# Optimization experiments

Hardware: AMD Instinct MI355X
Metric: run time of the kernel (lower is better)

The kernel has to match this reference:

```python
import jax, jax.numpy as jnp
import numpy as np

N = 50000      # nodes
E = 800000     # edges (avg degree 16)
IN_DIM = 128
H = 64         # hidden (GINSmall default)
C = 2          # n_classes
G = 64         # number of graphs in batch


def setup_inputs() -> dict:
    key = jax.random.key(0)
    ks = jax.random.split(key, 16)
    s = 0.05
    inp = {
        "x": jax.random.normal(ks[0], (N, IN_DIM), dtype=jnp.float32),
        "edge_index": jax.random.randint(ks[1], (2, E), 0, N, dtype=jnp.int64),
        "batch": jnp.sort(jax.random.randint(ks[2], (N,), 0, G, dtype=jnp.int64)),
        # conv 0 MLP
        "W1_0": jax.random.normal(ks[3], (IN_DIM, H), dtype=jnp.float32) * s,
        "b1_0": jnp.zeros((H,), jnp.float32),
        "W2_0": jax.random.normal(ks[4], (H, H), dtype=jnp.float32) * s,
        "b2_0": jnp.zeros((H,), jnp.float32),
        # conv 1 MLP
        "W1_1": jax.random.normal(ks[5], (H, H), dtype=jnp.float32) * s,
        "b1_1": jnp.zeros((H,), jnp.float32),
        "W2_1": jax.random.normal(ks[6], (H, H), dtype=jnp.float32) * s,
        "b2_1": jnp.zeros((H,), jnp.float32),
        # conv 2 MLP
        "W1_2": jax.random.normal(ks[7], (H, H), dtype=jnp.float32) * s,
        "b1_2": jnp.zeros((H,), jnp.float32),
        "W2_2": jax.random.normal(ks[8], (H, H), dtype=jnp.float32) * s,
        "b2_2": jnp.zeros((H,), jnp.float32),
        # readout
        "Wl": jax.random.normal(ks[9], (H, C), dtype=jnp.float32) * s,
        "bl": jnp.zeros((C,), jnp.float32),
    }
    return inp


def _gin_conv(h, src, dst, W1, b1, W2, b2):
    # GINConv with eps=0: MLP(h_i + sum_{j->i} h_j)
    agg = jax.ops.segment_sum(h[src], dst, num_segments=N)  # [N, d]
    z = h + agg
    return jnp.maximum(z @ W1 + b1, 0.0) @ W2 + b2


def reference(x, edge_index, batch,
              W1_0, b1_0, W2_0, b2_0,
              W1_1, b1_1, W2_1, b2_1,
              W1_2, b1_2, W2_2, b2_2,
              Wl, bl):
    src, dst = edge_index[0], edge_index[1]  # PyG: messages flow src -> dst
    params = [(W1_0, b1_0, W2_0, b2_0),
              (W1_1, b1_1, W2_1, b2_1),
              (W1_2, b1_2, W2_2, b2_2)]
    h = x
    for (W1, b1, W2, b2) in params:
        h = _gin_conv(h, src, dst, W1, b1, W2, b2)
        h = jnp.maximum(h, 0.0)  # ReLU; dropout is identity at inference
    # global mean pool over graph ids
    sums = jax.ops.segment_sum(h, batch, num_segments=G)          # [G, H]
    cnt = jax.ops.segment_sum(jnp.ones((N,), h.dtype), batch, num_segments=G)
    g = sums / jnp.maximum(cnt, 1.0)[:, None]
    out = g @ Wl + bl
    return out, g
```

## Files before the change

kernel.cpp:

```cpp
#include <hip/hip_runtime.h>

typedef unsigned short ushort_t;
typedef __attribute__((ext_vector_type(8))) short short8;
typedef __attribute__((ext_vector_type(4))) float f32x4;

__device__ inline float bflo(unsigned int u) { return __uint_as_float(u << 16); }
__device__ inline float bfhi(unsigned int u) { return __uint_as_float(u & 0xFFFF0000u); }
__device__ inline unsigned short f2bf(float f) {
    unsigned int u = __float_as_uint(f);
    return (unsigned short)((u + 0x7FFFu + ((u >> 16) & 1u)) >> 16);
}
__device__ inline unsigned int pk(float a, float b) {
    return (unsigned int)f2bf(a) | ((unsigned int)f2bf(b) << 16);
}

union U16B { uint4 u; short8 s; };

#define HB 512

__global__ __launch_bounds__(256) void gemm_hist(const float* __restrict__ x,
                                                 const float* __restrict__ W1,
                                                 ushort_t* __restrict__ Y, int n,
                                                 const int* __restrict__ dst,
                                                 int* __restrict__ deg,
                                                 int* __restrict__ rank, int E) {
    if (blockIdx.x < HB) {
        for (int e = blockIdx.x * 256 + threadIdx.x; e < E; e += HB * 256)
            rank[e] = atomicAdd(&deg[dst[e]], 1);
        return;
    }
    __shared__ ushort_t w1f[4][4][64][8];
    __shared__ ushort_t ybuf[64][72];
    for (int i = threadIdx.x; i < 8192; i += 256) {
        int j = i & 7, lane = (i >> 3) & 63, ct = (i >> 9) & 3, ks = (i >> 11) & 3;
        int k = ks * 32 + ((lane >> 4) << 3) + j;
        int c = ct * 16 + (lane & 15);
        w1f[ks][ct][lane][j] = f2bf(W1[k * 64 + c]);
    }
    __syncthreads();
    int w = threadIdx.x >> 6, lane = threadIdx.x & 63;
    int row0 = (blockIdx.x - HB) * 64;
    int arow = row0 + w * 16 + (lane & 15);
    if (arow >= n) arow = n - 1;
    const float* xr = x + (size_t)arow * 128;
    int k0base = (lane >> 4) << 3;

    f32x4 acc[4] = {{0,0,0,0},{0,0,0,0},{0,0,0,0},{0,0,0,0}};
#pragma unroll
    for (int ks = 0; ks < 4; ks++) {
        int k0 = ks * 32 + k0base;
        float4 aa = *(const float4*)(xr + k0);
        float4 ab = *(const float4*)(xr + k0 + 4);
        U16B af;
        af.u.x = pk(aa.x, aa.y);
        af.u.y = pk(aa.z, aa.w);
        af.u.z = pk(ab.x, ab.y);
        af.u.w = pk(ab.z, ab.w);
#pragma unroll
        for (int ct = 0; ct < 4; ct++) {
            short8 bf = *(const short8*)&w1f[ks][ct][lane][0];
            acc[ct] = __builtin_amdgcn_mfma_f32_16x16x32_bf16(af.s, bf, acc[ct], 0, 0, 0);
        }
    }
#pragma unroll
    for (int ct = 0; ct < 4; ct++)
#pragma unroll
        for (int r = 0; r < 4; r++)
            ybuf[w * 16 + ((lane >> 4) << 2) + r][ct * 16 + (lane & 15)] = f2bf(acc[ct][r]);
    __syncthreads();
    int row = threadIdx.x >> 2, seg = threadIdx.x & 3;
    if (row0 + row < n) {
        const uint4* p = (const uint4*)&ybuf[row][seg * 16];
        uint4 v0 = p[0], v1 = p[1];
        uint4* q = (uint4*)(Y + (size_t)(row0 + row) * 64 + seg * 16);
        q[0] = v0; q[1] = v1;
    }
}

__global__ __launch_bounds__(256) void scan_all(const int* __restrict__ deg,
                                                int* __restrict__ rowptr,
                                                int* __restrict__ aggr,
                                                int* __restrict__ flags, int n) {
    __shared__ int sdata[256];
    __shared__ int sagg[64];
    int b = blockIdx.x;
    int t = threadIdx.x;
    int base = b * 1024 + t * 4;
    int v[4]; int s = 0;
#pragma unroll
    for (int k = 0; k < 4; k++) { int i = base + k; v[k] = (i < n) ? deg[i] : 0; s += v[k]; }
    sdata[t] = s;
    __syncthreads();
    for (int off = 1; off < 256; off <<= 1) {
        int x = 0;
        if (t >= off) x = sdata[t - off];
        __syncthreads();
        if (t >= off) sdata[t] += x;
        __syncthreads();
    }
    int ex = sdata[t] - s;
    if (t == 255) {
        aggr[b] = sdata[255];
        __threadfence();
        atomicExch(&flags[b], 1);
    }
    if (t < 64) { while (atomicAdd(&flags[t], 0) == 0) {} }
    __syncthreads();
    if (t < 64) sagg[t] = aggr[t];
    __syncthreads();
    int bp = 0;
    for (int i = 0; i < b; i++) bp += sagg[i];
    int off = bp + ex;
#pragma unroll
    for (int k = 0; k < 4; k++) {
        int i = base + k;
        if (i < n) { rowptr[i] = off; off += v[k]; }
    }
    if (b == 63 && t == 255) rowptr[n] = bp + sdata[255];
}

__global__ __launch_bounds__(256) void fill_range(const int* __restrict__ src,
                                                  const int* __restrict__ dst,
                                                  const int* __restrict__ rank,
                                                  const int* __restrict__ rowptr,
                                                  int* __restrict__ col, int E, int CE) {
    int range = blockIdx.x & 7;
    int sub = blockIdx.x >> 3;
    int e0 = sub * CE;
    int e1 = min(e0 + CE, E);
    for (int e = e0 + threadIdx.x; e < e1; e += 256) {
        int d = dst[e];
        if ((d >> 13) == range) col[rowptr[d] + rank[e]] = src[e];
    }
}

template <int HASNEXT>
__global__ __launch_bounds__(256) void gfuse(const ushort_t* __restrict__ Y,
                                             const int* __restrict__ rowptr,
                                             const int* __restrict__ col,
                                             const float* __restrict__ b1,
                                             const float* __restrict__ W2,
                                             const float* __restrict__ b2,
                                             const float* __restrict__ Wn,
                                             ushort_t* __restrict__ Yn,
                                             const int* __restrict__ batch,
                                             float* __restrict__ sums, int n) {
    __shared__ ushort_t w2f[2][4][64][8];
    __shared__ ushort_t wnf[HASNEXT ? 2 : 1][4][64][8];
    __shared__ ushort_t st[64][72];
    __shared__ float vbuf[HASNEXT ? 1 : 64][65];
    __shared__ float b1s[64], b2s[64];
    for (int i = threadIdx.x; i < 4096; i += 256) {
        int j = i & 7, lane = (i >> 3) & 63, ct = (i >> 9) & 3, ks = (i >> 11) & 1;
        int k = ks * 32 + ((lane >> 4) << 3) + j;
        int c = ct * 16 + (lane & 15);
        w2f[ks][ct][lane][j] = f2bf(W2[k * 64 + c]);
        if (HASNEXT) wnf[ks][ct][lane][j] = f2bf(Wn[k * 64 + c]);
    }
    if (threadIdx.x < 64) { b1s[threadIdx.x] = b1[threadIdx.x]; b2s[threadIdx.x] = b2[threadIdx.x]; }
    __syncthreads();

    int row0 = blockIdx.x * 64;

    {
        int lr = threadIdx.x >> 2;
        int q  = threadIdx.x & 3;
        int gnode = row0 + lr;
        uint4 o0, o1;
        if (gnode < n) {
            const ushort_t* yb = Y + (size_t)gnode * 64 + q * 16;
            uint4 v0 = *(const uint4*)yb;
            uint4 v1 = *(const uint4*)(yb + 8);
            float ga[16];
            ga[0]=bflo(v0.x); ga[1]=bfhi(v0.x); ga[2]=bflo(v0.y); ga[3]=bfhi(v0.y);
            ga[4]=bflo(v0.z); ga[5]=bfhi(v0.z); ga[6]=bflo(v0.w); ga[7]=bfhi(v0.w);
            ga[8]=bflo(v1.x); ga[9]=bfhi(v1.x); ga[10]=bflo(v1.y); ga[11]=bfhi(v1.y);
            ga[12]=bflo(v1.z); ga[13]=bfhi(v1.z); ga[14]=bflo(v1.w); ga[15]=bfhi(v1.w);
            int e = rowptr[gnode], e1 = rowptr[gnode + 1];
            while (e + 1 < e1) {
                const ushort_t* p0 = Y + (size_t)col[e] * 64 + q * 16;
                const ushort_t* p1 = Y + (size_t)col[e + 1] * 64 + q * 16;
                uint4 a0 = *(const uint4*)p0, a1 = *(const uint4*)(p0 + 8);
                uint4 c0 = *(const uint4*)p1, c1 = *(const uint4*)(p1 + 8);
                ga[0]+=bflo(a0.x)+bflo(c0.x); ga[1]+=bfhi(a0.x)+bfhi(c0.x);
                ga[2]+=bflo(a0.y)+bflo(c0.y); ga[3]+=bfhi(a0.y)+bfhi(c0.y);
                ga[4]+=bflo(a0.z)+bflo(c0.z); ga[5]+=bfhi(a0.z)+bfhi(c0.z);
                ga[6]+=bflo(a0.w)+bflo(c0.w); ga[7]+=bfhi(a0.w)+bfhi(c0.w);
                ga[8]+=bflo(a1.x)+bflo(c1.x); ga[9]+=bfhi(a1.x)+bfhi(c1.x);
                ga[10]+=bflo(a1.y)+bflo(c1.y); ga[11]+=bfhi(a1.y)+bfhi(c1.y);
                ga[12]+=bflo(a1.z)+bflo(c1.z); ga[13]+=bfhi(a1.z)+bfhi(c1.z);
                ga[14]+=bflo(a1.w)+bflo(c1.w); ga[15]+=bfhi(a1.w)+bfhi(c1.w);
                e += 2;
            }
            if (e < e1) {
                const ushort_t* p0 = Y + (size_t)col[e] * 64 + q * 16;
                uint4 a0 = *(const uint4*)p0, a1 = *(const uint4*)(p0 + 8);
                ga[0]+=bflo(a0.x); ga[1]+=bfhi(a0.x); ga[2]+=bflo(a0.y); ga[3]+=bfhi(a0.y);
                ga[4]+=bflo(a0.z); ga[5]+=bfhi(a0.z); ga[6]+=bflo(a0.w); ga[7]+=bfhi(a0.w);
                ga[8]+=bflo(a1.x); ga[9]+=bfhi(a1.x); ga[10]+=bflo(a1.y); ga[11]+=bfhi(a1.y);
                ga[12]+=bflo(a1.z); ga[13]+=bfhi(a1.z); ga[14]+=bflo(a1.w); ga[15]+=bfhi(a1.w);
            }
            int d0 = q * 16;
#pragma unroll
            for (int j = 0; j < 16; j++) ga[j] = fmaxf(ga[j] + b1s[d0 + j], 0.0f);
            o0.x = pk(ga[0], ga[1]);  o0.y = pk(ga[2], ga[3]);
            o0.z = pk(ga[4], ga[5]);  o0.w = pk(ga[6], ga[7]);
            o1.x = pk(ga[8], ga[9]);  o1.y = pk(ga[10], ga[11]);
            o1.z = pk(ga[12], ga[13]); o1.w = pk(ga[14], ga[15]);
        } else {
            o0 = make_uint4(0, 0, 0, 0); o1 = o0;
        }
        *(uint4*)&st[lr][q * 16] = o0;
        *(uint4*)&st[lr][q * 16 + 8] = o1;
    }
    __syncthreads();

    int w = threadIdx.x >> 6, lane = threadIdx.x & 63;
    int k0base = (lane >> 4) << 3;
    f32x4 acc[4] = {{0,0,0,0},{0,0,0,0},{0,0,0,0},{0,0,0,0}};
#pragma unroll
    for (int ks = 0; ks < 2; ks++) {
        short8 af = *(const short8*)&st[w * 16 + (lane & 15)][ks * 32 + k0base];
#pragma unroll
        for (int ct = 0; ct < 4; ct++) {
            short8 bf = *(const short8*)&w2f[ks][ct][lane][0];
            acc[ct] = __builtin_amdgcn_mfma_f32_16x16x32_bf16(af, bf, acc[ct], 0, 0, 0);
        }
    }
    __syncthreads();

    int colb = lane & 15;
    if (HASNEXT) {
#pragma unroll
        for (int ct = 0; ct < 4; ct++)
#pragma unroll
            for (int r = 0; r < 4; r++) {
                float v = fmaxf(acc[ct][r] + b2s[ct * 16 + colb], 0.0f);
                st[w * 16 + ((lane >> 4) << 2) + r][ct * 16 + colb] = f2bf(v);
            }
        __syncthreads();
        f32x4 acc2[4] = {{0,0,0,0},{0,0,0,0},{0,0,0,0},{0,0,0,0}};
#pragma unroll
        for (int ks = 0; ks < 2; ks++) {
            short8 af2 = *(const short8*)&st[w * 16 + (lane & 15)][ks * 32 + k0base];
#pragma unroll
            for (int ct = 0; ct < 4; ct++) {
                short8 bf = *(const short8*)&wnf[ks][ct][lane][0];
                acc2[ct] = __builtin_amdgcn_mfma_f32_16x16x32_bf16(af2, bf, acc2[ct], 0, 0, 0);
            }
        }
        __syncthreads();
#pragma unroll
        for (int ct = 0; ct < 4; ct++)
#pragma unroll
            for (int r = 0; r < 4; r++)
                st[w * 16 + ((lane >> 4) << 2) + r][ct * 16 + colb] = f2bf(acc2[ct][r]);
        __syncthreads();
        int row = threadIdx.x >> 2, seg = threadIdx.x & 3;
        if (row0 + row < n) {
            const uint4* p = (const uint4*)&st[row][seg * 16];
            uint4 v0 = p[0], v1 = p[1];
            uint4* qp = (uint4*)(Yn + (size_t)(row0 + row) * 64 + seg * 16);
            qp[0] = v0; qp[1] = v1;
        }
    } else {
#pragma unroll
        for (int ct = 0; ct < 4; ct++)
#pragma unroll
            for (int r = 0; r < 4; r++) {
                float v = fmaxf(acc[ct][r] + b2s[ct * 16 + colb], 0.0f);
                vbuf[w * 16 + ((lane >> 4) << 2) + r][ct * 16 + colb] = v;
            }
        __syncthreads();
        int j  = threadIdx.x & 63;
        int i0 = (threadIdx.x >> 6) * 16;
        int cur = -1; float a = 0.0f;
        for (int i = i0; i < i0 + 16; i++) {
            int row = row0 + i;
            if (row >= n) break;
            int b = batch[row];
            if (b != cur) {
                if (cur >= 0) atomicAdd(&sums[cur * 64 + j], a);
                cur = b; a = 0.0f;
            }
            a += vbuf[i][j];
        }
        if (cur >= 0) atomicAdd(&sums[cur * 64 + j], a);
    }
}

__global__ __launch_bounds__(64) void finalize_kernel(const float* __restrict__ sums,
                                                      const int* __restrict__ batch, int n,
                                                      const float* __restrict__ Wl,
                                                      const float* __restrict__ bl,
                                                      float* __restrict__ out, int G) {
    int g = blockIdx.x;
    int j = threadIdx.x;
    __shared__ float gs[64];
    int lo = 0, hi = n;
    while (lo < hi) { int m = (lo + hi) >> 1; if (batch[m] < g) lo = m + 1; else hi = m; }
    int lo2 = lo, hi2 = n;
    while (lo2 < hi2) { int m = (lo2 + hi2) >> 1; if (batch[m] < g + 1) lo2 = m + 1; else hi2 = m; }
    float c = (float)max(lo2 - lo, 1);
    float v = sums[g * 64 + j] / c;
    gs[j] = v;
    out[G * 2 + g * 64 + j] = v;
    __syncthreads();
    if (j < 2) {
        float acc = bl[j];
#pragma unroll
        for (int k = 0; k < 64; k++) acc += gs[k] * Wl[k * 2 + j];
        out[g * 2 + j] = acc;
    }
}

extern "C" void kernel_launch(void* const* d_in, const int* in_sizes, int n_in,
                              void* d_out, int out_size, void* d_ws, size_t ws_size,
                              hipStream_t stream) {
    const float* x     = (const float*)d_in[0];
    const int*   ei    = (const int*)d_in[1];
    const int*   batch = (const int*)d_in[2];
    const float* W1_0 = (const float*)d_in[3];
    const float* b1_0 = (const float*)d_in[4];
    const float* W2_0 = (const float*)d_in[5];
    const float* b2_0 = (const float*)d_in[6];
    const float* W1_1 = (const float*)d_in[7];
    const float* b1_1 = (const float*)d_in[8];
    const float* W2_1 = (const float*)d_in[9];
    const float* b2_1 = (const float*)d_in[10];
    const float* W1_2 = (const float*)d_in[11];
    const float* b1_2 = (const float*)d_in[12];
    const float* W2_2 = (const float*)d_in[13];
    const float* b2_2 = (const float*)d_in[14];
    const float* Wl   = (const float*)d_in[15];
    const float* bl   = (const float*)d_in[16];

    const int N = in_sizes[0] / 128;
    const int E = in_sizes[1] / 2;
    const int G = out_size / 66;
    const int* src = ei;
    const int* dst = ei + E;
    float* out = (float*)d_out;

    ushort_t* Y   = (ushort_t*)d_ws;
    ushort_t* Y2  = Y + (size_t)N * 64;
    float* sums   = (float*)(Y2 + (size_t)N * 64);
    int*   deg    = (int*)(sums + (size_t)G * 64);
    int*   flags  = deg + N;
    int*   rowptr = flags + 64;
    int*   col    = rowptr + (N + 1);
    int*   rank   = col + E;
    int*   aggr   = rank + E;

    hipMemsetAsync(sums, 0, ((size_t)G * 64 + N + 64) * sizeof(int), stream);

    const int mblk = (N + 63) / 64;

    gemm_hist<<<HB + mblk, 256, 0, stream>>>(x, W1_0, Y, N, dst, deg, rank, E);
    scan_all<<<64, 256, 0, stream>>>(deg, rowptr, aggr, flags, N);
    const int SUBS = 64;
    const int CE = (E + SUBS - 1) / SUBS;
    fill_range<<<8 * SUBS, 256, 0, stream>>>(src, dst, rank, rowptr, col, E, CE);

    gfuse<1><<<mblk, 256, 0, stream>>>(Y, rowptr, col, b1_0, W2_0, b2_0, W1_1, Y2, nullptr, nullptr, N);
    gfuse<1><<<mblk, 256, 0, stream>>>(Y2, rowptr, col, b1_1, W2_1, b2_1, W1_2, Y, nullptr, nullptr, N);
    gfuse<0><<<mblk, 256, 0, stream>>>(Y, rowptr, col, b1_2, W2_2, b2_2, nullptr, nullptr, batch, sums, N);
    finalize_kernel<<<G, 64, 0, stream>>>(sums, batch, N, Wl, bl, out, G);
}
```

Before: 173.9 us.

## Partition CSR neighbor lists by source half to localize gather accesses

```diff
diff --git a/kernel.cpp b/kernel.cpp
--- a/kernel.cpp
+++ b/kernel.cpp
@@ -21,12 +21,16 @@
 __global__ __launch_bounds__(256) void gemm_hist(const float* __restrict__ x,
                                                  const float* __restrict__ W1,
                                                  ushort_t* __restrict__ Y, int n,
+                                                 const int* __restrict__ src,
                                                  const int* __restrict__ dst,
                                                  int* __restrict__ deg,
-                                                 int* __restrict__ rank, int E) {
+                                                 int* __restrict__ rank, int E, int HALF) {
     if (blockIdx.x < HB) {
-        for (int e = blockIdx.x * 256 + threadIdx.x; e < E; e += HB * 256)
-            rank[e] = atomicAdd(&deg[dst[e]], 1);
+        for (int e = blockIdx.x * 256 + threadIdx.x; e < E; e += HB * 256) {
+            int d = dst[e];
+            int off = (src[e] >= HALF) ? n : 0;
+            rank[e] = atomicAdd(&deg[d + off], 1);
+        }
         return;
     }
     __shared__ ushort_t w1f[4][4][64][8];
@@ -88,7 +92,11 @@
     int base = b * 1024 + t * 4;
     int v[4]; int s = 0;
 #pragma unroll
-    for (int k = 0; k < 4; k++) { int i = base + k; v[k] = (i < n) ? deg[i] : 0; s += v[k]; }
+    for (int k = 0; k < 4; k++) {
+        int i = base + k;
+        v[k] = (i < n) ? deg[i] + deg[n + i] : 0;
+        s += v[k];
+    }
     sdata[t] = s;
     __syncthreads();
     for (int off = 1; off < 256; off <<= 1) {
@@ -123,14 +131,19 @@
                                                   const int* __restrict__ dst,
                                                   const int* __restrict__ rank,
                                                   const int* __restrict__ rowptr,
-                                                  int* __restrict__ col, int E, int CE) {
+                                                  const int* __restrict__ deg,
+                                                  int* __restrict__ col, int E, int CE, int HALF) {
     int range = blockIdx.x & 7;
     int sub = blockIdx.x >> 3;
     int e0 = sub * CE;
     int e1 = min(e0 + CE, E);
     for (int e = e0 + threadIdx.x; e < e1; e += 256) {
         int d = dst[e];
-        if ((d >> 13) == range) col[rowptr[d] + rank[e]] = src[e];
+        if ((d >> 13) == range) {
+            int s = src[e];
+            int base = rowptr[d] + ((s >= HALF) ? deg[d] : 0);
+            col[base + rank[e]] = s;
+        }
     }
 }
 
@@ -138,6 +151,7 @@
 __global__ __launch_bounds__(256) void gfuse(const ushort_t* __restrict__ Y,
                                              const int* __restrict__ rowptr,
                                              const int* __restrict__ col,
+                                             const int* __restrict__ degA,
                                              const float* __restrict__ b1,
                                              const float* __restrict__ W2,
                                              const float* __restrict__ b2,
@@ -176,29 +190,35 @@
             ga[4]=bflo(v0.z); ga[5]=bfhi(v0.z); ga[6]=bflo(v0.w); ga[7]=bfhi(v0.w);
             ga[8]=bflo(v1.x); ga[9]=bfhi(v1.x); ga[10]=bflo(v1.y); ga[11]=bfhi(v1.y);
             ga[12]=bflo(v1.z); ga[13]=bfhi(v1.z); ga[14]=bflo(v1.w); ga[15]=bfhi(v1.w);
-            int e = rowptr[gnode], e1 = rowptr[gnode + 1];
-            while (e + 1 < e1) {
-                const ushort_t* p0 = Y + (size_t)col[e] * 64 + q * 16;
-                const ushort_t* p1 = Y + (size_t)col[e + 1] * 64 + q * 16;
-                uint4 a0 = *(const uint4*)p0, a1 = *(const uint4*)(p0 + 8);
-                uint4 c0 = *(const uint4*)p1, c1 = *(const uint4*)(p1 + 8);
-                ga[0]+=bflo(a0.x)+bflo(c0.x); ga[1]+=bfhi(a0.x)+bfhi(c0.x);
-                ga[2]+=bflo(a0.y)+bflo(c0.y); ga[3]+=bfhi(a0.y)+bfhi(c0.y);
-                ga[4]+=bflo(a0.z)+bflo(c0.z); ga[5]+=bfhi(a0.z)+bfhi(c0.z);
-                ga[6]+=bflo(a0.w)+bflo(c0.w); ga[7]+=bfhi(a0.w)+bfhi(c0.w);
-                ga[8]+=bflo(a1.x)+bflo(c1.x); ga[9]+=bfhi(a1.x)+bfhi(c1.x);
-                ga[10]+=bflo(a1.y)+bflo(c1.y); ga[11]+=bfhi(a1.y)+bfhi(c1.y);
-                ga[12]+=bflo(a1.z)+bflo(c1.z); ga[13]+=bfhi(a1.z)+bfhi(c1.z);
-                ga[14]+=bflo(a1.w)+bflo(c1.w); ga[15]+=bfhi(a1.w)+bfhi(c1.w);
-                e += 2;
-            }
-            if (e < e1) {
-                const ushort_t* p0 = Y + (size_t)col[e] * 64 + q * 16;
-                uint4 a0 = *(const uint4*)p0, a1 = *(const uint4*)(p0 + 8);
-                ga[0]+=bflo(a0.x); ga[1]+=bfhi(a0.x); ga[2]+=bflo(a0.y); ga[3]+=bfhi(a0.y);
-                ga[4]+=bflo(a0.z); ga[5]+=bfhi(a0.z); ga[6]+=bflo(a0.w); ga[7]+=bfhi(a0.w);
-                ga[8]+=bflo(a1.x); ga[9]+=bfhi(a1.x); ga[10]+=bflo(a1.y); ga[11]+=bfhi(a1.y);
-                ga[12]+=bflo(a1.z); ga[13]+=bfhi(a1.z); ga[14]+=bflo(a1.w); ga[15]+=bfhi(a1.w);
+            int r0 = rowptr[gnode], r1 = rowptr[gnode + 1];
+            int sp = r0 + degA[gnode];
+#pragma unroll 1
+            for (int p = 0; p < 2; p++) {
+                int e  = p ? sp : r0;
+                int ed = p ? r1 : sp;
+                while (e + 1 < ed) {
+                    const ushort_t* p0 = Y + (size_t)col[e] * 64 + q * 16;
+                    const ushort_t* p1 = Y + (size_t)col[e + 1] * 64 + q * 16;
+                    uint4 a0 = *(const uint4*)p0, a1 = *(const uint4*)(p0 + 8);
+                    uint4 c0 = *(const uint4*)p1, c1 = *(const uint4*)(p1 + 8);
+                    ga[0]+=bflo(a0.x)+bflo(c0.x); ga[1]+=bfhi(a0.x)+bfhi(c0.x);
+                    ga[2]+=bflo(a0.y)+bflo(c0.y); ga[3]+=bfhi(a0.y)+bfhi(c0.y);
+                    ga[4]+=bflo(a0.z)+bflo(c0.z); ga[5]+=bfhi(a0.z)+bfhi(c0.z);
+                    ga[6]+=bflo(a0.w)+bflo(c0.w); ga[7]+=bfhi(a0.w)+bfhi(c0.w);
+                    ga[8]+=bflo(a1.x)+bflo(c1.x); ga[9]+=bfhi(a1.x)+bfhi(c1.x);
+                    ga[10]+=bflo(a1.y)+bflo(c1.y); ga[11]+=bfhi(a1.y)+bfhi(c1.y);
+                    ga[12]+=bflo(a1.z)+bflo(c1.z); ga[13]+=bfhi(a1.z)+bfhi(c1.z);
+                    ga[14]+=bflo(a1.w)+bflo(c1.w); ga[15]+=bfhi(a1.w)+bfhi(c1.w);
+                    e += 2;
+                }
+                if (e < ed) {
+                    const ushort_t* p0 = Y + (size_t)col[e] * 64 + q * 16;
+                    uint4 a0 = *(const uint4*)p0, a1 = *(const uint4*)(p0 + 8);
+                    ga[0]+=bflo(a0.x); ga[1]+=bfhi(a0.x); ga[2]+=bflo(a0.y); ga[3]+=bfhi(a0.y);
+                    ga[4]+=bflo(a0.z); ga[5]+=bfhi(a0.z); ga[6]+=bflo(a0.w); ga[7]+=bfhi(a0.w);
+                    ga[8]+=bflo(a1.x); ga[9]+=bfhi(a1.x); ga[10]+=bflo(a1.y); ga[11]+=bfhi(a1.y);
+                    ga[12]+=bflo(a1.z); ga[13]+=bfhi(a1.z); ga[14]+=bflo(a1.w); ga[15]+=bfhi(a1.w);
+                }
             }
             int d0 = q * 16;
 #pragma unroll
@@ -341,29 +361,30 @@
     const int* src = ei;
     const int* dst = ei + E;
     float* out = (float*)d_out;
+    const int HALF = N / 2;
 
     ushort_t* Y   = (ushort_t*)d_ws;
     ushort_t* Y2  = Y + (size_t)N * 64;
     float* sums   = (float*)(Y2 + (size_t)N * 64);
     int*   deg    = (int*)(sums + (size_t)G * 64);
-    int*   flags  = deg + N;
+    int*   flags  = deg + 2 * (size_t)N;
     int*   rowptr = flags + 64;
     int*   col    = rowptr + (N + 1);
     int*   rank   = col + E;
     int*   aggr   = rank + E;
 
-    hipMemsetAsync(sums, 0, ((size_t)G * 64 + N + 64) * sizeof(int), stream);
+    hipMemsetAsync(sums, 0, ((size_t)G * 64 + 2 * (size_t)N + 64) * sizeof(int), stream);
 
     const int mblk = (N + 63) / 64;
 
-    gemm_hist<<<HB + mblk, 256, 0, stream>>>(x, W1_0, Y, N, dst, deg, rank, E);
+    gemm_hist<<<HB + mblk, 256, 0, stream>>>(x, W1_0, Y, N, src, dst, deg, rank, E, HALF);
     scan_all<<<64, 256, 0, stream>>>(deg, rowptr, aggr, flags, N);
     const int SUBS = 64;
     const int CE = (E + SUBS - 1) / SUBS;
-    fill_range<<<8 * SUBS, 256, 0, stream>>>(src, dst, rank, rowptr, col, E, CE);
-
-    gfuse<1><<<mblk, 256, 0, stream>>>(Y, rowptr, col, b1_0, W2_0, b2_0, W1_1, Y2, nullptr, nullptr, N);
-    gfuse<1><<<mblk, 256, 0, stream>>>(Y2, rowptr, col, b1_1, W2_1, b2_1, W1_2, Y, nullptr, nullptr, N);
-    gfuse<0><<<mblk, 256, 0, stream>>>(Y, rowptr, col, b1_2, W2_2, b2_2, nullptr, nullptr, batch, sums, N);
+    fill_range<<<8 * SUBS, 256, 0, stream>>>(src, dst, rank, rowptr, deg, col, E, CE, HALF);
+
+    gfuse<1><<<mblk, 256, 0, stream>>>(Y, rowptr, col, deg, b1_0, W2_0, b2_0, W1_1, Y2, nullptr, nullptr, N);
+    gfuse<1><<<mblk, 256, 0, stream>>>(Y2, rowptr, col, deg, b1_1, W2_1, b2_1, W1_2, Y, nullptr, nullptr, N);
+    gfuse<0><<<mblk, 256, 0, stream>>>(Y, rowptr, col, deg, b1_2, W2_2, b2_2, nullptr, nullptr, batch, sums, N);
     finalize_kernel<<<G, 64, 0, stream>>>(sums, batch, N, Wl, bl, out, G);
 }
```

Result: slower. 186.0 us (+6.9%).

## Fuse CSR scan and column fill into one kernel with flag-based handoff

Applied to the files above, without the earlier changes.

```diff
diff --git a/kernel.cpp b/kernel.cpp
--- a/kernel.cpp
+++ b/kernel.cpp
@@ -17,6 +17,7 @@
 union U16B { uint4 u; short8 s; };
 
 #define HB 512
+#define SUBS 192
 
 __global__ __launch_bounds__(256) void gemm_hist(const float* __restrict__ x,
                                                  const float* __restrict__ W1,
@@ -77,60 +78,71 @@
     }
 }
 
-__global__ __launch_bounds__(256) void scan_all(const int* __restrict__ deg,
-                                                int* __restrict__ rowptr,
-                                                int* __restrict__ aggr,
-                                                int* __restrict__ flags, int n) {
-    __shared__ int sdata[256];
-    __shared__ int sagg[64];
-    int b = blockIdx.x;
+__global__ __launch_bounds__(256) void scan_fill(const int* __restrict__ deg,
+                                                 int* __restrict__ rowptr,
+                                                 int* __restrict__ aggr,
+                                                 int* __restrict__ flags,
+                                                 int* __restrict__ flags2,
+                                                 const int* __restrict__ src,
+                                                 const int* __restrict__ dst,
+                                                 const int* __restrict__ rank,
+                                                 int* __restrict__ col,
+                                                 int n, int E, int CE, int RB) {
     int t = threadIdx.x;
-    int base = b * 1024 + t * 4;
-    int v[4]; int s = 0;
-#pragma unroll
-    for (int k = 0; k < 4; k++) { int i = base + k; v[k] = (i < n) ? deg[i] : 0; s += v[k]; }
-    sdata[t] = s;
-    __syncthreads();
-    for (int off = 1; off < 256; off <<= 1) {
-        int x = 0;
-        if (t >= off) x = sdata[t - off];
-        __syncthreads();
-        if (t >= off) sdata[t] += x;
-        __syncthreads();
-    }
-    int ex = sdata[t] - s;
-    if (t == 255) {
-        aggr[b] = sdata[255];
+    if (blockIdx.x < 64) {
+        __shared__ int sdata[256];
+        __shared__ int sagg[64];
+        int b = blockIdx.x;
+        int base = b * 1024 + t * 4;
+        int v[4]; int s = 0;
+#pragma unroll
+        for (int k = 0; k < 4; k++) { int i = base + k; v[k] = (i < n) ? deg[i] : 0; s += v[k]; }
+        sdata[t] = s;
+        __syncthreads();
+        for (int off = 1; off < 256; off <<= 1) {
+            int x = 0;
+            if (t >= off) x = sdata[t - off];
+            __syncthreads();
+            if (t >= off) sdata[t] += x;
+            __syncthreads();
+        }
+        int ex = sdata[t] - s;
+        if (t == 255) {
+            aggr[b] = sdata[255];
+            __threadfence();
+            atomicExch(&flags[b], 1);
+        }
+        if (t < 64) { while (atomicAdd(&flags[t], 0) == 0) {} }
+        __syncthreads();
+        if (t < 64) sagg[t] = aggr[t];
+        __syncthreads();
+        int bp = 0;
+        for (int i = 0; i < b; i++) bp += sagg[i];
+        int off = bp + ex;
+#pragma unroll
+        for (int k = 0; k < 4; k++) {
+            int i = base + k;
+            if (i < n) { rowptr[i] = off; off += v[k]; }
+        }
+        if (b == 63 && t == 255) rowptr[n] = bp + sdata[255];
+        __syncthreads();
         __threadfence();
-        atomicExch(&flags[b], 1);
-    }
-    if (t < 64) { while (atomicAdd(&flags[t], 0) == 0) {} }
-    __syncthreads();
-    if (t < 64) sagg[t] = aggr[t];
-    __syncthreads();
-    int bp = 0;
-    for (int i = 0; i < b; i++) bp += sagg[i];
-    int off = bp + ex;
-#pragma unroll
-    for (int k = 0; k < 4; k++) {
-        int i = base + k;
-        if (i < n) { rowptr[i] = off; off += v[k]; }
-    }
-    if (b == 63 && t == 255) rowptr[n] = bp + sdata[255];
-}
-
-__global__ __launch_bounds__(256) void fill_range(const int* __restrict__ src,
-                                                  const int* __restrict__ dst,
-                                                  const int* __restrict__ rank,
-                                                  const int* __restrict__ rowptr,
-                                                  int* __restrict__ col, int E, int CE) {
-    int range = blockIdx.x & 7;
-    int sub = blockIdx.x >> 3;
-    int e0 = sub * CE;
-    int e1 = min(e0 + CE, E);
-    for (int e = e0 + threadIdx.x; e < e1; e += 256) {
-        int d = dst[e];
-        if ((d >> 13) == range) col[rowptr[d] + rank[e]] = src[e];
+        if (t == 0) atomicExch(&flags2[b], 1);
+    } else {
+        if (t < 64) { while (atomicAdd(&flags2[t], 0) == 0) {} }
+        __syncthreads();
+        int fb = blockIdx.x - 64;
+        int range = fb & 7;
+        int sub = fb >> 3;
+        int e0 = sub * CE;
+        int e1 = min(e0 + CE, E);
+        int lo = range * RB;
+        int hi = lo + RB;
+#pragma unroll 4
+        for (int e = e0 + t; e < e1; e += 256) {
+            int d = dst[e];
+            if (d >= lo && d < hi) col[rowptr[d] + rank[e]] = src[e];
+        }
     }
 }
 
@@ -347,20 +359,21 @@
     float* sums   = (float*)(Y2 + (size_t)N * 64);
     int*   deg    = (int*)(sums + (size_t)G * 64);
     int*   flags  = deg + N;
-    int*   rowptr = flags + 64;
+    int*   flags2 = flags + 64;
+    int*   rowptr = flags2 + 64;
     int*   col    = rowptr + (N + 1);
     int*   rank   = col + E;
     int*   aggr   = rank + E;
 
-    hipMemsetAsync(sums, 0, ((size_t)G * 64 + N + 64) * sizeof(int), stream);
+    hipMemsetAsync(sums, 0, ((size_t)G * 64 + N + 128) * sizeof(int), stream);
 
     const int mblk = (N + 63) / 64;
+    const int CE = (E + SUBS - 1) / SUBS;
+    const int RB = (N + 7) / 8;
 
     gemm_hist<<<HB + mblk, 256, 0, stream>>>(x, W1_0, Y, N, dst, deg, rank, E);
-    scan_all<<<64, 256, 0, stream>>>(deg, rowptr, aggr, flags, N);
-    const int SUBS = 64;
-    const int CE = (E + SUBS - 1) / SUBS;
-    fill_range<<<8 * SUBS, 256, 0, stream>>>(src, dst, rank, rowptr, col, E, CE);
+    scan_fill<<<64 + 8 * SUBS, 256, 0, stream>>>(deg, rowptr, aggr, flags, flags2,
+                                                 src, dst, rank, col, N, E, CE, RB);
 
     gfuse<1><<<mblk, 256, 0, stream>>>(Y, rowptr, col, b1_0, W2_0, b2_0, W1_1, Y2, nullptr, nullptr, N);
     gfuse<1><<<mblk, 256, 0, stream>>>(Y2, rowptr, col, b1_1, W2_1, b2_1, W1_2, Y, nullptr, nullptr, N);
```

Measured after the change: 169.1 us. -2.8%, faster.
